# Kernel optimization log

Hardware: AMD Instinct MI355X
Metric: run time of the kernel (lower is better)

## Reference

```python
import jax, jax.numpy as jnp
import numpy as np

INPUT_SIZE = 4
HIDDEN_SIZE = 4
SEQ_LEN = 2048
BATCH = 4096


def _lstm_layer(x, W_ih, W_hh, b_ih, b_hh):
    """Single-layer LSTM over x: [T, B, I]; PyTorch gate order (i, f, g, o)."""
    H = W_hh.shape[1]
    B = x.shape[1]
    # Precompute the input projection for all timesteps (one big GEMM).
    xg = jnp.einsum('tbi,gi->tbg', x, W_ih) + (b_ih + b_hh)  # [T, B, 4H]

    def step(carry, xg_t):
        h, c = carry
        gates = xg_t + h @ W_hh.T  # [B, 4H]
        i, f, g, o = jnp.split(gates, 4, axis=-1)
        i = jax.nn.sigmoid(i)
        f = jax.nn.sigmoid(f)
        g = jnp.tanh(g)
        o = jax.nn.sigmoid(o)
        c = f * c + i * g
        h = o * jnp.tanh(c)
        return (h, c), h

    h0 = jnp.zeros((B, H), x.dtype)
    c0 = jnp.zeros((B, H), x.dtype)
    _, ys = jax.lax.scan(step, (h0, c0), xg)
    return ys  # [T, B, H]


def setup_inputs() -> dict:
    key = jax.random.key(0)
    ks = jax.random.split(key, 9)
    bound = 1.0 / np.sqrt(HIDDEN_SIZE)  # torch LSTM init: U(-1/sqrt(H), 1/sqrt(H))

    def u(k, shape):
        return jax.random.uniform(k, shape, jnp.float32, -bound, bound)

    x = jax.random.normal(ks[0], (SEQ_LEN, BATCH, INPUT_SIZE), jnp.float32)
    return {
        'x': x,
        'W_ih0': u(ks[1], (4 * HIDDEN_SIZE, INPUT_SIZE)),
        'W_hh0': u(ks[2], (4 * HIDDEN_SIZE, HIDDEN_SIZE)),
        'b_ih0': u(ks[3], (4 * HIDDEN_SIZE,)),
        'b_hh0': u(ks[4], (4 * HIDDEN_SIZE,)),
        'W_ih1': u(ks[5], (4 * HIDDEN_SIZE, HIDDEN_SIZE)),
        'W_hh1': u(ks[6], (4 * HIDDEN_SIZE, HIDDEN_SIZE)),
        'b_ih1': u(ks[7], (4 * HIDDEN_SIZE,)),
        'b_hh1': u(ks[8], (4 * HIDDEN_SIZE,)),
    }


def reference(x, W_ih0, W_hh0, b_ih0, b_hh0, W_ih1, W_hh1, b_ih1, b_hh1):
    h1 = _lstm_layer(x, W_ih0, W_hh0, b_ih0, b_hh0)
    h2 = _lstm_layer(h1, W_ih1, W_hh1, b_ih1, b_hh1)
    return h2  # [T, B, H], matching `x, _ = self.lstm(x); return x`
```

## Files before the change

kernel.cpp:

```cpp
#include <hip/hip_runtime.h>

#define SEQ_T   2048
#define BATCH_N 4096
#define LOG2E   1.4426950408889634f
#define K_SEG   8
#define NSEG    (SEQ_T / K_SEG)

#define DPPF(v, ctrl) __int_as_float(__builtin_amdgcn_mov_dpp(__float_as_int(v), (ctrl), 0xF, 0xF, true))
#define RHM 0x141
#define MIR 0x140

__global__ __launch_bounds__(256, 2) void lstm2_split(
    const float* __restrict__ x,
    const float* __restrict__ Wih0, const float* __restrict__ Whh0,
    const float* __restrict__ bih0, const float* __restrict__ bhh0,
    const float* __restrict__ Wih1, const float* __restrict__ Whh1,
    const float* __restrict__ bih1, const float* __restrict__ bhh1,
    float* __restrict__ out)
{
    __shared__ float ring[16][8][4];

    const int wv    = threadIdx.x >> 6;
    const int lane  = threadIdx.x & 63;
    const int cpos  = lane >> 4;
    const int g16   = lane & 15;
    const int u     = g16 >> 2;
    const int r     = g16 & 3;
    const int row   = r * 4 + u;
    const bool isA  = (wv < 2);
    const int lch   = (wv & 1) * 4 + cpos;
    const int chain = blockIdx.x * 8 + lch;

    const float srow = (r == 2) ? (-2.0f * LOG2E) : (-LOG2E);
    float win[4], whh[4];
    float bb;
    if (isA) {
#pragma unroll
        for (int d = 0; d < 4; ++d) {
            win[d] = Wih0[row * 4 + d]       * srow;
            whh[d] = Whh0[row * 4 + (u ^ d)] * srow;
        }
        bb = (bih0[row] + bhh0[row]) * srow;
    } else {
#pragma unroll
        for (int d = 0; d < 4; ++d) {
            win[d] = Wih1[row * 4 + (u ^ d)] * srow;
            whh[d] = Whh1[row * 4 + (u ^ d)] * srow;
        }
        bb = (bih1[row] + bhh1[row]) * srow;
    }
    const float csc = -2.0f * LOG2E;
    float ka = (r == 2) ? 2.0f * csc : 1.0f;
    float kb = (r == 2) ? -1.0f * csc : 0.0f;

    const char* __restrict__ xb = (const char*)x;
    char* __restrict__ ob = (char*)out;

    float h = 0.f, ha = 0.f, hb2 = 0.f, hc = 0.f;
    float cs = 0.f;

    if (isA) {
        const unsigned xhome = (unsigned)chain * 16u;
        float4 xreg[K_SEG];
        unsigned xoff = xhome;
#pragma unroll
        for (int i = 0; i < K_SEG; ++i) {
            xreg[i] = *(const float4*)(xb + xoff);
            xoff += 65536u;
        }
        for (int seg = 0; seg <= NSEG; ++seg) {
            __syncthreads();
            if (seg < NSEG) {
                const int slotbase = (seg * K_SEG) & 15;
                const bool pf = (seg + 1 < NSEG);
#pragma unroll
                for (int i = 0; i < K_SEG; ++i) {
                    const float4 xv = xreg[i];
                    if (pf) {
                        xreg[i] = *(const float4*)(xb + xoff);
                        xoff += 65536u;
                    }
                    float acc = fmaf(win[0], xv.x, fmaf(win[1], xv.y,
                                fmaf(win[2], xv.z, fmaf(win[3], xv.w, bb))));
                    acc = fmaf(whh[0], h, fmaf(whh[1], ha,
                          fmaf(whh[2], hb2, fmaf(whh[3], hc, acc))));
                    float e = __builtin_amdgcn_exp2f(acc);
                    float s = __builtin_amdgcn_rcpf(1.0f + e);
                    float a = fmaf(ka, s, kb);
                    float iv = DPPF(a, 0x00), fv = DPPF(a, 0x55);
                    float gv = DPPF(a, 0xAA), ov = DPPF(a, 0xFF);
                    cs = fmaf(fv, cs, iv * gv);
                    float z = __builtin_amdgcn_exp2f(cs);
                    float t2 = fmaf(2.0f, __builtin_amdgcn_rcpf(1.0f + z), -1.0f);
                    h  = ov * t2;
                    ha = DPPF(h, RHM);
                    hc = DPPF(h, MIR);
                    hb2 = DPPF(ha, MIR);
                    if (r == 0) ring[slotbase + i][lch][u] = h;
                }
            }
        }
    } else {
        unsigned ooff = (unsigned)(chain * 16 + u * 4);
        for (int seg = 0; seg <= NSEG; ++seg) {
            __syncthreads();
            if (seg > 0) {
                const int slotbase = ((seg - 1) * K_SEG) & 15;
                float hreg[K_SEG];
#pragma unroll
                for (int i = 0; i < K_SEG; ++i)
                    hreg[i] = ring[slotbase + i][lch][u];
#pragma unroll
                for (int i = 0; i < K_SEG; ++i) {
                    const float X = hreg[i];
                    float Xa = DPPF(X, RHM);
                    float Xc = DPPF(X, MIR);
                    float Xb = DPPF(Xa, MIR);
                    float acc = fmaf(win[0], X, fmaf(win[1], Xa,
                                fmaf(win[2], Xb, fmaf(win[3], Xc, bb))));
                    acc = fmaf(whh[0], h, fmaf(whh[1], ha,
                          fmaf(whh[2], hb2, fmaf(whh[3], hc, acc))));
                    float e = __builtin_amdgcn_exp2f(acc);
                    float s = __builtin_amdgcn_rcpf(1.0f + e);
                    float a = fmaf(ka, s, kb);
                    float iv = DPPF(a, 0x00), fv = DPPF(a, 0x55);
                    float gv = DPPF(a, 0xAA), ov = DPPF(a, 0xFF);
                    cs = fmaf(fv, cs, iv * gv);
                    float z = __builtin_amdgcn_exp2f(cs);
                    float t2 = fmaf(2.0f, __builtin_amdgcn_rcpf(1.0f + z), -1.0f);
                    h  = ov * t2;
                    ha = DPPF(h, RHM);
                    hc = DPPF(h, MIR);
                    hb2 = DPPF(ha, MIR);
                    if (r == 0) *(float*)(ob + ooff) = h;
                    ooff += 65536u;
                }
            }
        }
    }
}

extern "C" void kernel_launch(void* const* d_in, const int* in_sizes, int n_in,
                              void* d_out, int out_size, void* d_ws, size_t ws_size,
                              hipStream_t stream) {
    const float* x    = (const float*)d_in[0];
    const float* Wih0 = (const float*)d_in[1];
    const float* Whh0 = (const float*)d_in[2];
    const float* bih0 = (const float*)d_in[3];
    const float* bhh0 = (const float*)d_in[4];
    const float* Wih1 = (const float*)d_in[5];
    const float* Whh1 = (const float*)d_in[6];
    const float* bih1 = (const float*)d_in[7];
    const float* bhh1 = (const float*)d_in[8];
    float* out = (float*)d_out;

    dim3 grid(512), block(256);
    hipLaunchKernelGGL(lstm2_split, grid, block, 0, stream,
                       x, Wih0, Whh0, bih0, bhh0, Wih1, Whh1, bih1, bhh1, out);
}
```

Before: 284.5 us.

## Halve block size, double segment length, use float4 LDS reads for layer-1 input

Blocks shrink to one producer wave (layer 0) and one consumer wave (layer 1), so the grid doubles to 1024 blocks of 128 threads. Segments grow to 16 timesteps in a double-buffered LDS ring, which halves the number of __syncthreads barriers. Layer 1 now reads all four hidden values as a float4 from LDS instead of gathering them through DPP shuffles. The x prefetch becomes a rolling 8-deep buffer with a clamped address. The intent is less barrier overhead and fewer cross-lane ops, at the cost of more register pressure from the longer unrolled loop.

```diff
diff --git a/kernel.cpp b/kernel.cpp
--- a/kernel.cpp
+++ b/kernel.cpp
@@ -3,14 +3,14 @@
 #define SEQ_T   2048
 #define BATCH_N 4096
 #define LOG2E   1.4426950408889634f
-#define K_SEG   8
+#define K_SEG   16
 #define NSEG    (SEQ_T / K_SEG)
 
 #define DPPF(v, ctrl) __int_as_float(__builtin_amdgcn_mov_dpp(__float_as_int(v), (ctrl), 0xF, 0xF, true))
 #define RHM 0x141
 #define MIR 0x140
 
-__global__ __launch_bounds__(256, 2) void lstm2_split(
+__global__ __launch_bounds__(128, 2) void lstm2_split(
     const float* __restrict__ x,
     const float* __restrict__ Wih0, const float* __restrict__ Whh0,
     const float* __restrict__ bih0, const float* __restrict__ bhh0,
@@ -18,7 +18,7 @@
     const float* __restrict__ bih1, const float* __restrict__ bhh1,
     float* __restrict__ out)
 {
-    __shared__ float ring[16][8][4];
+    __shared__ float ring[32][4][4];
 
     const int wv    = threadIdx.x >> 6;
     const int lane  = threadIdx.x & 63;
@@ -27,13 +27,11 @@
     const int u     = g16 >> 2;
     const int r     = g16 & 3;
     const int row   = r * 4 + u;
-    const bool isA  = (wv < 2);
-    const int lch   = (wv & 1) * 4 + cpos;
-    const int chain = blockIdx.x * 8 + lch;
+    const int chain = blockIdx.x * 4 + cpos;
+    const bool isA  = (wv == 0);
 
     const float srow = (r == 2) ? (-2.0f * LOG2E) : (-LOG2E);
-    float win[4], whh[4];
-    float bb;
+    float win[4], whh[4], bb;
     if (isA) {
 #pragma unroll
         for (int d = 0; d < 4; ++d) {
@@ -44,14 +42,14 @@
     } else {
 #pragma unroll
         for (int d = 0; d < 4; ++d) {
-            win[d] = Wih1[row * 4 + (u ^ d)] * srow;
+            win[d] = Wih1[row * 4 + d]       * srow;
             whh[d] = Whh1[row * 4 + (u ^ d)] * srow;
         }
         bb = (bih1[row] + bhh1[row]) * srow;
     }
     const float csc = -2.0f * LOG2E;
-    float ka = (r == 2) ? 2.0f * csc : 1.0f;
-    float kb = (r == 2) ? -1.0f * csc : 0.0f;
+    const float ka = (r == 2) ? 2.0f * csc : 1.0f;
+    const float kb = (r == 2) ? -csc       : 0.0f;
 
     const char* __restrict__ xb = (const char*)x;
     char* __restrict__ ob = (char*)out;
@@ -59,44 +57,47 @@
     float h = 0.f, ha = 0.f, hb2 = 0.f, hc = 0.f;
     float cs = 0.f;
 
+    auto cell = [&](float acc) {
+        acc = fmaf(whh[0], h, fmaf(whh[1], ha,
+              fmaf(whh[2], hb2, fmaf(whh[3], hc, acc))));
+        float e = __builtin_amdgcn_exp2f(acc);
+        float s = __builtin_amdgcn_rcpf(1.0f + e);
+        float a = fmaf(ka, s, kb);
+        float iv = DPPF(a, 0x00), fv = DPPF(a, 0x55);
+        float gv = DPPF(a, 0xAA), ov = DPPF(a, 0xFF);
+        cs = fmaf(fv, cs, iv * gv);
+        float z  = __builtin_amdgcn_exp2f(cs);
+        float t2 = fmaf(2.0f, __builtin_amdgcn_rcpf(1.0f + z), -1.0f);
+        h  = ov * t2;
+        ha = DPPF(h, RHM);
+        hc = DPPF(h, MIR);
+        hb2 = DPPF(ha, MIR);
+    };
+
     if (isA) {
         const unsigned xhome = (unsigned)chain * 16u;
-        float4 xreg[K_SEG];
+        const unsigned XCL   = xhome + 2047u * 65536u;
+        float4 xbuf[8];
         unsigned xoff = xhome;
 #pragma unroll
-        for (int i = 0; i < K_SEG; ++i) {
-            xreg[i] = *(const float4*)(xb + xoff);
+        for (int i = 0; i < 8; ++i) {
+            xbuf[i] = *(const float4*)(xb + xoff);
             xoff += 65536u;
         }
         for (int seg = 0; seg <= NSEG; ++seg) {
             __syncthreads();
             if (seg < NSEG) {
-                const int slotbase = (seg * K_SEG) & 15;
-                const bool pf = (seg + 1 < NSEG);
+                float (*slot)[4] = ring[(seg & 1) * K_SEG];
 #pragma unroll
                 for (int i = 0; i < K_SEG; ++i) {
-                    const float4 xv = xreg[i];
-                    if (pf) {
-                        xreg[i] = *(const float4*)(xb + xoff);
-                        xoff += 65536u;
-                    }
+                    const float4 xv = xbuf[i & 7];
+                    unsigned off = (xoff < XCL) ? xoff : XCL;
+                    xbuf[i & 7] = *(const float4*)(xb + off);
+                    xoff += 65536u;
                     float acc = fmaf(win[0], xv.x, fmaf(win[1], xv.y,
                                 fmaf(win[2], xv.z, fmaf(win[3], xv.w, bb))));
-                    acc = fmaf(whh[0], h, fmaf(whh[1], ha,
-                          fmaf(whh[2], hb2, fmaf(whh[3], hc, acc))));
-                    float e = __builtin_amdgcn_exp2f(acc);
-                    float s = __builtin_amdgcn_rcpf(1.0f + e);
-                    float a = fmaf(ka, s, kb);
-                    float iv = DPPF(a, 0x00), fv = DPPF(a, 0x55);
-                    float gv = DPPF(a, 0xAA), ov = DPPF(a, 0xFF);
-                    cs = fmaf(fv, cs, iv * gv);
-                    float z = __builtin_amdgcn_exp2f(cs);
-                    float t2 = fmaf(2.0f, __builtin_amdgcn_rcpf(1.0f + z), -1.0f);
-                    h  = ov * t2;
-                    ha = DPPF(h, RHM);
-                    hc = DPPF(h, MIR);
-                    hb2 = DPPF(ha, MIR);
-                    if (r == 0) ring[slotbase + i][lch][u] = h;
+                    cell(acc);
+                    if (r == 0) slot[i * 4 + cpos][u] = h;
                 }
             }
         }
@@ -105,35 +106,22 @@
         for (int seg = 0; seg <= NSEG; ++seg) {
             __syncthreads();
             if (seg > 0) {
-                const int slotbase = ((seg - 1) * K_SEG) & 15;
-                float hreg[K_SEG];
+                const float (*slot)[4] = ring[((seg - 1) & 1) * K_SEG];
+                float4 hr[8];
 #pragma unroll
-                for (int i = 0; i < K_SEG; ++i)
-                    hreg[i] = ring[slotbase + i][lch][u];
+                for (int hf = 0; hf < 2; ++hf) {
 #pragma unroll
-                for (int i = 0; i < K_SEG; ++i) {
-                    const float X = hreg[i];
-                    float Xa = DPPF(X, RHM);
-                    float Xc = DPPF(X, MIR);
-                    float Xb = DPPF(Xa, MIR);
-                    float acc = fmaf(win[0], X, fmaf(win[1], Xa,
-                                fmaf(win[2], Xb, fmaf(win[3], Xc, bb))));
-                    acc = fmaf(whh[0], h, fmaf(whh[1], ha,
-                          fmaf(whh[2], hb2, fmaf(whh[3], hc, acc))));
-                    float e = __builtin_amdgcn_exp2f(acc);
-                    float s = __builtin_amdgcn_rcpf(1.0f + e);
-                    float a = fmaf(ka, s, kb);
-                    float iv = DPPF(a, 0x00), fv = DPPF(a, 0x55);
-                    float gv = DPPF(a, 0xAA), ov = DPPF(a, 0xFF);
-                    cs = fmaf(fv, cs, iv * gv);
-                    float z = __builtin_amdgcn_exp2f(cs);
-                    float t2 = fmaf(2.0f, __builtin_amdgcn_rcpf(1.0f + z), -1.0f);
-                    h  = ov * t2;
-                    ha = DPPF(h, RHM);
-                    hc = DPPF(h, MIR);
-                    hb2 = DPPF(ha, MIR);
-                    if (r == 0) *(float*)(ob + ooff) = h;
-                    ooff += 65536u;
+                    for (int s = 0; s < 8; ++s)
+                        hr[s] = *(const float4*)&slot[(hf * 8 + s) * 4 + cpos][0];
+#pragma unroll
+                    for (int i = 0; i < 8; ++i) {
+                        const float4 X = hr[i];
+                        float acc = fmaf(win[0], X.x, fmaf(win[1], X.y,
+                                    fmaf(win[2], X.z, fmaf(win[3], X.w, bb))));
+                        cell(acc);
+                        if (r == 0) *(float*)(ob + ooff) = h;
+                        ooff += 65536u;
+                    }
                 }
             }
         }
@@ -154,7 +142,7 @@
     const float* bhh1 = (const float*)d_in[8];
     float* out = (float*)d_out;
 
-    dim3 grid(512), block(256);
+    dim3 grid(1024), block(128);
     hipLaunchKernelGGL(lstm2_split, grid, block, 0, stream,
                        x, Wih0, Whh0, bih0, bhh0, Wih1, Whh1, bih1, bhh1, out);
 }
```

Result: faster. 258.8 us (-9.0%).
